# Performance work log

Measured on AMD Instinct MI355X. Metric: run time of the kernel, lower is better.

Reference implementation:

```python
import jax, jax.numpy as jnp
import numpy as np

KL_ALPHA = 0.3
MSE_WEIGHT = 1.0


def setup_inputs() -> dict:
    key = jax.random.key(0)
    ks = jax.random.split(key, 8)
    B, S, V = 4, 512, 32000
    logits = jax.random.normal(ks[0], (B, S + 1, V), dtype=jnp.float32)
    ref_logits = jax.random.normal(ks[1], (B, S + 1, V), dtype=jnp.float32)
    input_ids = jax.random.randint(ks[2], (B, S), 0, V, dtype=jnp.int32)
    attention_mask = jnp.ones((B, S), dtype=jnp.int32)
    word_ids = jnp.sort(jax.random.randint(ks[3], (B, S), 0, S, dtype=jnp.int32), axis=1)
    word_lengths = jax.random.randint(ks[4], (B, S), 0, 12, dtype=jnp.int32)
    log_unigram_frequencies = jax.random.normal(ks[5], (B, S), dtype=jnp.float32)
    labels = jax.random.normal(ks[6], (B, S), dtype=jnp.float32)
    W_head = jax.random.normal(ks[7], (3,), dtype=jnp.float32) * 0.1
    b_head = jnp.zeros((1,), dtype=jnp.float32)
    return dict(logits=logits, ref_logits=ref_logits, input_ids=input_ids,
                attention_mask=attention_mask, word_ids=word_ids,
                word_lengths=word_lengths,
                log_unigram_frequencies=log_unigram_frequencies,
                labels=labels, W_head=W_head, b_head=b_head)


def reference(logits, ref_logits, input_ids, attention_mask, word_ids,
              word_lengths, log_unigram_frequencies, labels, W_head, b_head):
    B, S = input_ids.shape
    lp = jax.nn.log_softmax(logits, axis=-1)                       # [B,S+1,V]
    rlp = jax.lax.stop_gradient(jax.nn.log_softmax(ref_logits, axis=-1))

    # token surprisal = -log p(token_t | prefix): gather from shifted log-probs
    lp_shift = lp[:, :-1, :]                                       # [B,S,V]
    surprisal = -jnp.take_along_axis(lp_shift, input_ids[..., None], axis=2)[..., 0]

    # scatter_add token surprisal into word bins (masked tokens -> bin 0 with value 0)
    mask = word_ids != -1                                          # [B,S]
    masked_surp = surprisal * mask
    masked_wid = jnp.where(mask, word_ids, 0)
    rows = jnp.arange(B)[:, None]
    summed_surprisal = jnp.zeros((B, S), surprisal.dtype).at[rows, masked_wid].add(masked_surp)

    # vectorized per-token gather of word-level features (replaces the Python loop)
    valid = (word_ids >= 0) & (word_ids < S)
    safe = jnp.clip(word_ids, 0, S - 1)
    lens = jnp.take_along_axis(word_lengths, safe, axis=1)
    valid = valid & (lens != -1)
    exp_len = jnp.where(valid, lens.astype(jnp.float32), 0.0)
    exp_freq = jnp.where(valid, jnp.take_along_axis(log_unigram_frequencies, safe, axis=1), 0.0)

    # Linear(3,1) head on [surprisal, length, frequency]
    preds = summed_surprisal * W_head[0] + exp_len * W_head[1] + exp_freq * W_head[2] + b_head[0]

    # masked MSE over valid words (torch boolean extraction == masked mean)
    mask_words = (labels != -1.0).astype(jnp.float32)
    mse_loss = jnp.sum((labels - preds) ** 2 * mask_words) / jnp.sum(mask_words)
    loss = MSE_WEIGHT * mse_loss

    # KL divergence to frozen reference over masked tokens (log_target form)
    kl_mask = jnp.concatenate([jnp.zeros((B, 1), bool), mask[:, :-1]], axis=1).astype(jnp.float32)
    lp_s, rlp_s = lp[:, :-1, :], rlp[:, :-1, :]                    # [B,S,V]
    kl_tok = jnp.sum(jnp.exp(rlp_s) * (rlp_s - lp_s), axis=-1)     # [B,S]
    kl_loss = jnp.sum(kl_tok * kl_mask) / jnp.sum(kl_mask)

    # average log-prob of next tokens and delta vs reference
    shift_ids = input_ids[:, 1:]                                   # [B,S-1]
    ans_mask = attention_mask[:, 1:].astype(jnp.float32)
    g = jnp.take_along_axis(lp[:, :S - 1, :], shift_ids[..., None], axis=2)[..., 0]
    gr = jnp.take_along_axis(rlp[:, :S - 1, :], shift_ids[..., None], axis=2)[..., 0]
    avg_log_prob = jnp.sum(g * ans_mask) / jnp.sum(ans_mask)
    delta_log_prob = avg_log_prob - jnp.sum(gr * ans_mask) / jnp.sum(ans_mask)

    loss = loss + KL_ALPHA * kl_loss
    return loss, preds, mse_loss, kl_loss, avg_log_prob, delta_log_prob
```

## Files before the change

kernel.cpp:

```cpp
#include <hip/hip_runtime.h>
#include <math.h>

#define NB 4
#define NS 512
#define NV 32000
#define NROWS (NB * NS)
#define KL_ALPHA 0.3f

__device__ __forceinline__ void merge2(float& m, float& s, float om, float os) {
    float nm = fmaxf(m, om);
    s = s * __expf(m - nm) + os * __expf(om - nm);
    m = nm;
}
__device__ __forceinline__ void merge3(float& m, float& s, float& t, float om, float os, float ot) {
    float nm = fmaxf(m, om);
    float ea = __expf(m - nm), eb = __expf(om - nm);
    s = s * ea + os * eb;
    t = t * ea + ot * eb;
    m = nm;
}

__global__ __launch_bounds__(256) void krow(const float* __restrict__ logits,
                                            const float* __restrict__ ref_logits,
                                            const int* __restrict__ input_ids,
                                            float* __restrict__ logZx,
                                            float* __restrict__ logZy,
                                            float* __restrict__ klrow,
                                            float* __restrict__ surp,
                                            float* __restrict__ gval,
                                            float* __restrict__ grval) {
    const int row = blockIdx.x;
    const int b = row / NS, s = row - b * NS;
    const size_t base = (size_t)(b * (NS + 1) + s) * NV;
    const float4* __restrict__ x4 = (const float4*)(logits + base);
    const float4* __restrict__ y4 = (const float4*)(ref_logits + base);
    const int tid = threadIdx.x;

    float mx[4], sx[4], my[4], sy[4], ty[4];
#pragma unroll
    for (int j = 0; j < 4; ++j) { mx[j] = -INFINITY; sx[j] = 0.f; my[j] = -INFINITY; sy[j] = 0.f; ty[j] = 0.f; }

    for (int i = tid; i < NV / 4; i += 256) {
        float4 xv = x4[i];
        float4 yv = y4[i];
        float xs[4] = {xv.x, xv.y, xv.z, xv.w};
        float ys[4] = {yv.x, yv.y, yv.z, yv.w};
#pragma unroll
        for (int j = 0; j < 4; ++j) {
            float xe = xs[j], ye = ys[j];
            float nmx = fmaxf(mx[j], xe);
            sx[j] = sx[j] * __expf(mx[j] - nmx) + __expf(xe - nmx);
            mx[j] = nmx;
            float nmy = fmaxf(my[j], ye);
            float a = __expf(my[j] - nmy);
            float e = __expf(ye - nmy);
            sy[j] = sy[j] * a + e;
            ty[j] = ty[j] * a + e * (ye - xe);
            my[j] = nmy;
        }
    }
    float Mx = mx[0], Sx = sx[0];
    float My = my[0], Sy = sy[0], Ty = ty[0];
#pragma unroll
    for (int j = 1; j < 4; ++j) {
        merge2(Mx, Sx, mx[j], sx[j]);
        merge3(My, Sy, Ty, my[j], sy[j], ty[j]);
    }
    for (int off = 32; off > 0; off >>= 1) {
        float oMx = __shfl_xor(Mx, off);
        float oSx = __shfl_xor(Sx, off);
        merge2(Mx, Sx, oMx, oSx);
        float oMy = __shfl_xor(My, off);
        float oSy = __shfl_xor(Sy, off);
        float oTy = __shfl_xor(Ty, off);
        merge3(My, Sy, Ty, oMy, oSy, oTy);
    }
    __shared__ float red[4][5];
    const int wave = tid >> 6, lane = tid & 63;
    if (lane == 0) {
        red[wave][0] = Mx; red[wave][1] = Sx;
        red[wave][2] = My; red[wave][3] = Sy; red[wave][4] = Ty;
    }
    __syncthreads();
    if (tid == 0) {
        for (int w = 1; w < 4; ++w) {
            merge2(Mx, Sx, red[w][0], red[w][1]);
            merge3(My, Sy, Ty, red[w][2], red[w][3], red[w][4]);
        }
        float lzx = Mx + __logf(Sx);
        float lzy = My + __logf(Sy);
        logZx[row] = lzx;
        logZy[row] = lzy;
        klrow[row] = Ty / Sy + lzx - lzy;
        int id0 = input_ids[b * NS + s];
        surp[row] = lzx - logits[base + id0];
        if (s < NS - 1) {
            int id1 = input_ids[b * NS + s + 1];
            gval[row]  = logits[base + id1] - lzx;
            grval[row] = ref_logits[base + id1] - lzy;
        } else {
            gval[row] = 0.f;
            grval[row] = 0.f;
        }
    }
}

__global__ __launch_bounds__(1024) void kfinal(const int* __restrict__ input_ids,
                                               const int* __restrict__ attention_mask,
                                               const int* __restrict__ word_ids,
                                               const int* __restrict__ word_lengths,
                                               const float* __restrict__ lufreq,
                                               const float* __restrict__ labels,
                                               const float* __restrict__ W_head,
                                               const float* __restrict__ b_head,
                                               const float* __restrict__ logZx,
                                               const float* __restrict__ logZy,
                                               const float* __restrict__ klrow,
                                               const float* __restrict__ surp,
                                               const float* __restrict__ gval,
                                               const float* __restrict__ grval,
                                               float* __restrict__ out) {
    __shared__ float summed[NROWS];
    const int tid = threadIdx.x;
    for (int p = tid; p < NROWS; p += 1024) summed[p] = 0.f;
    __syncthreads();
    for (int p = tid; p < NROWS; p += 1024) {
        int b = p / NS;
        int wid = word_ids[p];
        if (wid >= 0 && wid < NS) atomicAdd(&summed[b * NS + wid], surp[p]);
    }
    __syncthreads();

    const float W0 = W_head[0], W1 = W_head[1], W2 = W_head[2], bh = b_head[0];
    float mse_n = 0.f, mse_d = 0.f, kl_n = 0.f, kl_d = 0.f;
    float g_n = 0.f, gr_n = 0.f, g_d = 0.f;
    for (int p = tid; p < NROWS; p += 1024) {
        int b = p / NS, s = p - b * NS;
        int wid = word_ids[p];
        bool valid = (wid >= 0) && (wid < NS);
        int safe = wid < 0 ? 0 : (wid > NS - 1 ? NS - 1 : wid);
        int lens = word_lengths[b * NS + safe];
        valid = valid && (lens != -1);
        float el = valid ? (float)lens : 0.f;
        float ef = valid ? lufreq[b * NS + safe] : 0.f;
        float pred = summed[p] * W0 + el * W1 + ef * W2 + bh;
        out[1 + p] = pred;
        float lab = labels[p];
        float mw = (lab != -1.0f) ? 1.f : 0.f;
        float diff = lab - pred;
        mse_n += diff * diff * mw;
        mse_d += mw;
        float km = (s == 0) ? 0.f : ((word_ids[p - 1] != -1) ? 1.f : 0.f);
        kl_n += klrow[p] * km;
        kl_d += km;
        if (s < NS - 1) {
            float am = (float)attention_mask[b * NS + s + 1];
            g_n += gval[p] * am;
            gr_n += grval[p] * am;
            g_d += am;
        }
    }
    for (int off = 32; off > 0; off >>= 1) {
        mse_n += __shfl_xor(mse_n, off);
        mse_d += __shfl_xor(mse_d, off);
        kl_n  += __shfl_xor(kl_n, off);
        kl_d  += __shfl_xor(kl_d, off);
        g_n   += __shfl_xor(g_n, off);
        gr_n  += __shfl_xor(gr_n, off);
        g_d   += __shfl_xor(g_d, off);
    }
    __shared__ float r2[16][7];
    const int wave = tid >> 6, lane = tid & 63;
    if (lane == 0) {
        r2[wave][0] = mse_n; r2[wave][1] = mse_d;
        r2[wave][2] = kl_n;  r2[wave][3] = kl_d;
        r2[wave][4] = g_n;   r2[wave][5] = gr_n; r2[wave][6] = g_d;
    }
    __syncthreads();
    if (tid == 0) {
        float a0 = 0, a1 = 0, a2 = 0, a3 = 0, a4 = 0, a5 = 0, a6 = 0;
        for (int w = 0; w < 16; ++w) {
            a0 += r2[w][0]; a1 += r2[w][1]; a2 += r2[w][2]; a3 += r2[w][3];
            a4 += r2[w][4]; a5 += r2[w][5]; a6 += r2[w][6];
        }
        float mse = a0 / a1;
        float kl = a2 / a3;
        float loss = mse + KL_ALPHA * kl;
        float avg = a4 / a6;
        float delta = avg - a5 / a6;
        out[0] = loss;
        out[1 + NROWS] = mse;
        out[2 + NROWS] = kl;
        out[3 + NROWS] = avg;
        out[4 + NROWS] = delta;
    }
}

extern "C" void kernel_launch(void* const* d_in, const int* in_sizes, int n_in,
                              void* d_out, int out_size, void* d_ws, size_t ws_size,
                              hipStream_t stream) {
    const float* logits        = (const float*)d_in[0];
    const float* ref_logits    = (const float*)d_in[1];
    const int*   input_ids     = (const int*)d_in[2];
    const int*   attention_mask= (const int*)d_in[3];
    const int*   word_ids      = (const int*)d_in[4];
    const int*   word_lengths  = (const int*)d_in[5];
    const float* lufreq        = (const float*)d_in[6];
    const float* labels        = (const float*)d_in[7];
    const float* W_head        = (const float*)d_in[8];
    const float* b_head        = (const float*)d_in[9];
    float* out = (float*)d_out;
    float* ws = (float*)d_ws;

    float* logZx = ws;
    float* logZy = ws + NROWS;
    float* klrow = ws + 2 * NROWS;
    float* surp  = ws + 3 * NROWS;
    float* gvals = ws + 4 * NROWS;
    float* grvals= ws + 5 * NROWS;

    hipLaunchKernelGGL(krow, dim3(NROWS), dim3(256), 0, stream,
                       logits, ref_logits, input_ids,
                       logZx, logZy, klrow, surp, gvals, grvals);
    hipLaunchKernelGGL(kfinal, dim3(1), dim3(1024), 0, stream,
                       input_ids, attention_mask, word_ids, word_lengths,
                       lufreq, labels, W_head, b_head,
                       logZx, logZy, klrow, surp, gvals, grvals, out);
}
```

Baseline: 111.7 us.

## Replace online softmax with unshifted exp sums plus guarded rescaled fallback

Drops the per-element online max-rescaling in the row reduction and accumulates plain exp(x), exp(y) and exp(y)*(y-x) sums, tracking the max separately. If the row max exceeds a safe threshold, a second pass recomputes the sums with max subtraction. This removes two extra exponentials and the rescale multiplies per element, and simplifies the cross-lane merges to plain adds. It relies on the logits being bounded for the fast path; otherwise the fallback rereads the row.

```diff
diff --git a/kernel.cpp b/kernel.cpp
--- a/kernel.cpp
+++ b/kernel.cpp
@@ -6,19 +6,7 @@
 #define NV 32000
 #define NROWS (NB * NS)
 #define KL_ALPHA 0.3f
-
-__device__ __forceinline__ void merge2(float& m, float& s, float om, float os) {
-    float nm = fmaxf(m, om);
-    s = s * __expf(m - nm) + os * __expf(om - nm);
-    m = nm;
-}
-__device__ __forceinline__ void merge3(float& m, float& s, float& t, float om, float os, float ot) {
-    float nm = fmaxf(m, om);
-    float ea = __expf(m - nm), eb = __expf(om - nm);
-    s = s * ea + os * eb;
-    t = t * ea + ot * eb;
-    m = nm;
-}
+#define SAFE_MAX 60.0f
 
 __global__ __launch_bounds__(256) void krow(const float* __restrict__ logits,
                                             const float* __restrict__ ref_logits,
@@ -36,9 +24,10 @@
     const float4* __restrict__ y4 = (const float4*)(ref_logits + base);
     const int tid = threadIdx.x;
 
-    float mx[4], sx[4], my[4], sy[4], ty[4];
-#pragma unroll
-    for (int j = 0; j < 4; ++j) { mx[j] = -INFINITY; sx[j] = 0.f; my[j] = -INFINITY; sy[j] = 0.f; ty[j] = 0.f; }
+    float sx[4] = {0.f, 0.f, 0.f, 0.f};
+    float sy[4] = {0.f, 0.f, 0.f, 0.f};
+    float ty[4] = {0.f, 0.f, 0.f, 0.f};
+    float mx = -INFINITY, my = -INFINITY;
 
     for (int i = tid; i < NV / 4; i += 256) {
         float4 xv = x4[i];
@@ -48,50 +37,84 @@
 #pragma unroll
         for (int j = 0; j < 4; ++j) {
             float xe = xs[j], ye = ys[j];
-            float nmx = fmaxf(mx[j], xe);
-            sx[j] = sx[j] * __expf(mx[j] - nmx) + __expf(xe - nmx);
-            mx[j] = nmx;
-            float nmy = fmaxf(my[j], ye);
-            float a = __expf(my[j] - nmy);
-            float e = __expf(ye - nmy);
-            sy[j] = sy[j] * a + e;
-            ty[j] = ty[j] * a + e * (ye - xe);
-            my[j] = nmy;
-        }
-    }
-    float Mx = mx[0], Sx = sx[0];
-    float My = my[0], Sy = sy[0], Ty = ty[0];
-#pragma unroll
-    for (int j = 1; j < 4; ++j) {
-        merge2(Mx, Sx, mx[j], sx[j]);
-        merge3(My, Sy, Ty, my[j], sy[j], ty[j]);
-    }
+            mx = fmaxf(mx, xe);
+            my = fmaxf(my, ye);
+            float ex = __expf(xe);
+            float ey = __expf(ye);
+            sx[j] += ex;
+            sy[j] += ey;
+            ty[j] = fmaf(ey, ye - xe, ty[j]);
+        }
+    }
+    float Sx = (sx[0] + sx[1]) + (sx[2] + sx[3]);
+    float Sy = (sy[0] + sy[1]) + (sy[2] + sy[3]);
+    float Ty = (ty[0] + ty[1]) + (ty[2] + ty[3]);
+
     for (int off = 32; off > 0; off >>= 1) {
-        float oMx = __shfl_xor(Mx, off);
-        float oSx = __shfl_xor(Sx, off);
-        merge2(Mx, Sx, oMx, oSx);
-        float oMy = __shfl_xor(My, off);
-        float oSy = __shfl_xor(Sy, off);
-        float oTy = __shfl_xor(Ty, off);
-        merge3(My, Sy, Ty, oMy, oSy, oTy);
+        Sx += __shfl_xor(Sx, off);
+        Sy += __shfl_xor(Sy, off);
+        Ty += __shfl_xor(Ty, off);
+        mx = fmaxf(mx, __shfl_xor(mx, off));
+        my = fmaxf(my, __shfl_xor(my, off));
     }
     __shared__ float red[4][5];
     const int wave = tid >> 6, lane = tid & 63;
     if (lane == 0) {
-        red[wave][0] = Mx; red[wave][1] = Sx;
-        red[wave][2] = My; red[wave][3] = Sy; red[wave][4] = Ty;
-    }
-    __syncthreads();
+        red[wave][0] = Sx; red[wave][1] = Sy; red[wave][2] = Ty;
+        red[wave][3] = mx; red[wave][4] = my;
+    }
+    __syncthreads();
+    float tSx = 0.f, tSy = 0.f, tTy = 0.f, tMx = -INFINITY, tMy = -INFINITY;
+#pragma unroll
+    for (int w = 0; w < 4; ++w) {
+        tSx += red[w][0];
+        tSy += red[w][1];
+        tTy += red[w][2];
+        tMx = fmaxf(tMx, red[w][3]);
+        tMy = fmaxf(tMy, red[w][4]);
+    }
+
+    float lzx, lzy, klv;
+    if (tMx < SAFE_MAX && tMy < SAFE_MAX) {
+        lzx = __logf(tSx);
+        lzy = __logf(tSy);
+        klv = tTy / tSy + lzx - lzy;
+    } else {
+        float fsx = 0.f, fsy = 0.f, fty = 0.f;
+        for (int i = tid; i < NV / 4; i += 256) {
+            float4 xv = x4[i];
+            float4 yv = y4[i];
+            float xs[4] = {xv.x, xv.y, xv.z, xv.w};
+            float ys[4] = {yv.x, yv.y, yv.z, yv.w};
+#pragma unroll
+            for (int j = 0; j < 4; ++j) {
+                float xe = xs[j], ye = ys[j];
+                fsx += __expf(xe - tMx);
+                float ey = __expf(ye - tMy);
+                fsy += ey;
+                fty = fmaf(ey, ye - xe, fty);
+            }
+        }
+        for (int off = 32; off > 0; off >>= 1) {
+            fsx += __shfl_xor(fsx, off);
+            fsy += __shfl_xor(fsy, off);
+            fty += __shfl_xor(fty, off);
+        }
+        __syncthreads();
+        if (lane == 0) { red[wave][0] = fsx; red[wave][1] = fsy; red[wave][2] = fty; }
+        __syncthreads();
+        float gSx = 0.f, gSy = 0.f, gTy = 0.f;
+#pragma unroll
+        for (int w = 0; w < 4; ++w) { gSx += red[w][0]; gSy += red[w][1]; gTy += red[w][2]; }
+        lzx = tMx + __logf(gSx);
+        lzy = tMy + __logf(gSy);
+        klv = gTy / gSy + lzx - lzy;
+    }
+
     if (tid == 0) {
-        for (int w = 1; w < 4; ++w) {
-            merge2(Mx, Sx, red[w][0], red[w][1]);
-            merge3(My, Sy, Ty, red[w][2], red[w][3], red[w][4]);
-        }
-        float lzx = Mx + __logf(Sx);
-        float lzy = My + __logf(Sy);
         logZx[row] = lzx;
         logZy[row] = lzy;
-        klrow[row] = Ty / Sy + lzx - lzy;
+        klrow[row] = klv;
         int id0 = input_ids[b * NS + s];
         surp[row] = lzx - logits[base + id0];
         if (s < NS - 1) {
```

New measurement: 110.0 us. About the same (-1.6%).
